# Optimization experiments

Hardware: AMD Instinct MI355X
Metric: run time of the kernel (lower is better)

## Reference

```python
import jax, jax.numpy as jnp
from jax import lax
import numpy as np


def setup_inputs() -> dict:
    key = jax.random.key(0)
    ks = iter(jax.random.split(key, 48))

    def w(shape):
        fan = shape[0] if len(shape) == 2 else int(np.prod(shape[1:]))
        return jax.random.normal(next(ks), shape, jnp.float32) / np.sqrt(fan)

    def b(n):
        return jax.random.normal(next(ks), (n,), jnp.float32) * 0.01

    T = 16
    return dict(
        search=jax.random.normal(next(ks), (3, 383, 287), jnp.float32),
        exemplars=jax.random.normal(next(ks), (T, 3, 383, 287), jnp.float32),
        # AlexNet features (random-weight stand-in for pretrained)
        aw1=w((64, 3, 11, 11)), ab1=b(64),
        aw2=w((192, 64, 5, 5)), ab2=b(192),
        aw3=w((384, 192, 3, 3)), ab3=b(384),
        aw4=w((256, 384, 3, 3)), ab4=b(256),
        aw5=w((256, 256, 3, 3)), ab5=b(256),
        # conv_deconv: Conv1d(256,256,3,p=1) -> MaxPool1d(88) -> ConvTranspose1d(256,256,88)
        wcd=w((256, 256, 3)), bcd=b(256),
        wt=w((256, 256, 88)), bt=b(256),
        # st_gcn: GCN(256, 512, 256)
        ws1=w((256, 512)), bs1=b(512),
        ws2=w((512, 256)), bs2=b(256),
        # g, h: 1x1 Conv1d(256,256) == linear maps
        wg=w((256, 256)), bg=b(256),
        wh=w((256, 256)), bh=b(256),
        # ct_gcn: GCN(256, 384, 256)
        wc1=w((256, 384)), bc1=b(384),
        wc2=w((384, 256)), bc2=b(256),
    )


def _gct_forward(search, exemplars, aw1, ab1, aw2, ab2, aw3, ab3, aw4, ab4,
                 aw5, ab5, wcd, bcd, wt, bt, ws1, bs1, ws2, bs2,
                 wg, bg, wh, bh, wc1, bc1, wc2, bc2):
    f32 = jnp.float32

    def conv2d(x, w, bias, s, p):
        y = lax.conv_general_dilated(x, w, (s, s), [(p, p), (p, p)],
                                     dimension_numbers=('NCHW', 'OIHW', 'NCHW'))
        return y + bias[None, :, None, None]

    def maxpool(x):  # k=3, s=2, VALID (AlexNet pools)
        return lax.reduce_window(x, -jnp.inf, lax.max, (1, 1, 3, 3), (1, 1, 2, 2), 'VALID')

    def features(x):
        x = maxpool(jax.nn.relu(conv2d(x, aw1, ab1, 4, 2)))
        x = maxpool(jax.nn.relu(conv2d(x, aw2, ab2, 1, 2)))
        x = jax.nn.relu(conv2d(x, aw3, ab3, 1, 1))
        x = jax.nn.relu(conv2d(x, aw4, ab4, 1, 1))
        x = maxpool(jax.nn.relu(conv2d(x, aw5, ab5, 1, 1)))
        return x

    lrelu = lambda v: jax.nn.leaky_relu(v, 0.01)

    X = features(search[None])          # [1,256,11,8]
    Z = features(exemplars)             # [T,256,11,8]
    T = Z.shape[0]
    D = X.shape[1]                      # 256
    M = X.shape[2] * X.shape[3]         # 88
    Xf = X.reshape(D, M)                # [256,88]
    Zf = Z.reshape(T, D, M)             # [T,256,88]

    # conv_deconv branch: conv1d(k=3,p=1) -> global maxpool -> conv_transpose(k=M)
    xc = lax.conv_general_dilated(Xf[None], wcd, (1,), [(1, 1)],
                                  dimension_numbers=('NCH', 'OIH', 'NCH'))[0] + bcd[:, None]
    v = jnp.max(xc, axis=1)                              # [256]
    X_hat = jnp.einsum('i,iok->ok', v, wt) + bt[:, None]  # [256,88]

    # spatiotemporal graph: A[i+T*j, i+T*k]=1 for j!=k; self-loops for t!=0
    TM = T * M
    n = jnp.arange(TM)
    same_t = (n[:, None] % T) == (n[None, :] % T)
    diff_s = (n[:, None] // T) != (n[None, :] // T)
    A1 = (same_t & diff_s).astype(f32) + jnp.diag((n % T != 0).astype(f32))

    # st GCN over TM nodes (node n = t + T*m -> spatial-major flatten)
    nodes = Zf.transpose(2, 0, 1).reshape(TM, D)          # [TM,256]
    h1 = lrelu(A1 @ (nodes @ ws1) + bs1)                  # [TM,512]
    h2 = lrelu(A1 @ (h1 @ ws2) + bs2)                     # [TM,256]
    V1 = jnp.max(h2.reshape(M, T, D), axis=1).T           # temporal max-pool -> [256,88]

    # dynamic cross-track graph: pairwise g/h affinities + row softmax (fused)
    Vx = V1 + X_hat                                       # [256,88]
    G = wg @ Vx + bg[:, None]                             # [256,88]
    Hh = wh @ Vx + bh[:, None]                            # [256,88]
    A2 = jax.nn.softmax(Hh.T @ G, axis=1)                 # [88,88], A2[j,i]=g(i).h(j)

    # ct GCN
    xv = V1.T                                             # [88,256]
    c1 = lrelu(A2 @ (xv @ wc1) + bc1)                     # [88,384]
    V2 = lrelu(A2 @ (c1 @ wc2) + bc2).T                   # [256,88]

    # F.conv2d(X[1,256,11,8], V2[1,256,11,8]) -> full-overlap correlation = scalar
    R = jnp.sum(Xf * V2).reshape(1, 1, 1, 1)
    return R


def reference(search, exemplars, aw1, ab1, aw2, ab2, aw3, ab3, aw4, ab4,
              aw5, ab5, wcd, bcd, wt, bt, ws1, bs1, ws2, bs2,
              wg, bg, wh, bh, wc1, bc1, wc2, bc2):
    return _gct_forward(search, exemplars, aw1, ab1, aw2, ab2, aw3, ab3, aw4, ab4,
                        aw5, ab5, wcd, bcd, wt, bt, ws1, bs1, ws2, bs2,
                        wg, bg, wh, bh, wc1, bc1, wc2, bc2)
```

## Files before the change

### kernel.cpp

```cpp
#include <hip/hip_runtime.h>
#include <hip/hip_bf16.h>
#include <math.h>

#define BATCH 17
#define T_EX 16
#define H0 383
#define W0 287
#define C1 64
#define H1 95
#define W1 71
#define H1P 47
#define W1P 35
#define C2 192
#define H2P 23
#define W2P 17
#define C3 384
#define C45 256
#define H5P 11
#define W5P 8
#define DD 256
#define MM 88
#define TM 1408

#define HP1 389
#define WP1 292

typedef unsigned short ushort_t;
typedef __attribute__((ext_vector_type(8))) short short8;
typedef __attribute__((ext_vector_type(4))) float f32x4;

__device__ __forceinline__ float lrelu(float v) { return v > 0.f ? v : 0.01f * v; }

__device__ __forceinline__ ushort_t f2bf(float f) {
    unsigned int u = __float_as_uint(f);
    unsigned int r = (u + 0x7fffu + ((u >> 16) & 1u)) >> 16;
    return (ushort_t)r;
}
__device__ __forceinline__ float b2f(ushort_t b) {
    return __uint_as_float(((unsigned int)b) << 16);
}
__device__ __forceinline__ short8 ld16(const ushort_t* p) { return *(const short8*)p; }
__device__ __forceinline__ short8 ld2x8(const ushort_t* p) {
    union { uint2 u[2]; short8 s; } uu;
    uu.u[0] = *(const uint2*)p;
    uu.u[1] = *(const uint2*)(p + 4);
    return uu.s;
}
__device__ __forceinline__ void async_cp16(ushort_t* l, const ushort_t* g) {
    __builtin_amdgcn_global_load_lds(
        (const __attribute__((address_space(1))) void*)g,
        (__attribute__((address_space(3))) void*)l, 16, 0, 0);
}

__global__ void zfill_k(float4* __restrict__ p, int n4) {
    int idx = blockIdx.x * 256 + threadIdx.x;
    if (idx < n4) p[idx] = (float4){0.f, 0.f, 0.f, 0.f};
}

__global__ void prep1_k(const float* __restrict__ search, const float* __restrict__ exemp,
                        ushort_t* __restrict__ out) {
    int idx = blockIdx.x * 256 + threadIdx.x;
    if (idx >= BATCH * H0 * W0) return;
    int ix = idx % W0; int t = idx / W0;
    int iy = t % H0; int b = t / H0;
    const float* src = (b == 0) ? search : exemp + (size_t)(b - 1) * 3 * H0 * W0;
    const int hw = H0 * W0;
    float v0 = src[iy * W0 + ix];
    float v1 = src[hw + iy * W0 + ix];
    float v2 = src[2 * hw + iy * W0 + ix];
    ushort4 o;
    o.x = f2bf(v0); o.y = f2bf(v1); o.z = f2bf(v2); o.w = 0;
    *(ushort4*)&out[(((size_t)b * HP1 + iy + 2) * WP1 + ix + 2) * 4] = o;
}

__global__ void wprep_k(const float* __restrict__ w, ushort_t* __restrict__ out,
                        int KH, int KWl, int KWr, int CINl, int CINr,
                        int NKS, int nch) {
    int idx = blockIdx.x * 256 + threadIdx.x;
    if (idx >= nch) return;
    int c = idx & 255;
    int rest = idx >> 8;
    int ks = rest % NKS;
    int ocb = rest / NKS;
    int k8 = c >> 6, m = c & 63;
    int oc = ocb * 64 + m;
    int KWC = KWl * CINl;
    ushort_t* o = out + (size_t)idx * 8;
#pragma unroll
    for (int j = 0; j < 8; ++j) {
        int kg = ks * 32 + k8 * 8 + j;
        int ky = kg / KWC; int rem = kg - ky * KWC;
        int kx = rem / CINl; int ic = rem - kx * CINl;
        float v = 0.f;
        if (ky < KH && kx < KWr && ic < CINr)
            v = w[(((size_t)oc * CINr + ic) * KH + ky) * KWr + kx];
        o[j] = f2bf(v);
    }
}

__global__ void wprep_gemm_k(const float* __restrict__ ws1, const float* __restrict__ ws2,
                             const float* __restrict__ wcd, ushort_t* __restrict__ WS1T,
                             ushort_t* __restrict__ WS2T, ushort_t* __restrict__ WCDT) {
    int idx = blockIdx.x * 256 + threadIdx.x;
    const float* src; ushort_t* dst; int NKS, mode = 0, sa = 1, sk = 0, base;
    if (idx < 16384)       { src = ws1; dst = WS1T; NKS = 8;  sk = 512; base = idx; }
    else if (idx < 32768)  { src = ws2; dst = WS2T; NKS = 16; sk = 256; base = idx - 16384; }
    else if (idx < 57344)  { src = wcd; dst = WCDT; NKS = 24; mode = 1; base = idx - 32768; }
    else return;
    int c = base & 255;
    int rest = base >> 8;
    int ks = rest % NKS;
    int ocb = rest / NKS;
    int k8 = c >> 6, m = c & 63;
    int oc = ocb * 64 + m;
    ushort_t* o = dst + (size_t)base * 8;
#pragma unroll
    for (int j = 0; j < 8; ++j) {
        int kg = ks * 32 + k8 * 8 + j;
        float v;
        if (mode == 0) v = src[(size_t)oc * sa + (size_t)kg * sk];
        else           v = src[(size_t)oc * 768 + (kg & 255) * 3 + (kg >> 8)];
        o[j] = f2bf(v);
    }
}

template <int STRIDE, bool A16>
__global__ __launch_bounds__(256) void conv_mfma5(
    const ushort_t* __restrict__ inp, const ushort_t* __restrict__ wt,
    const float* __restrict__ bias, ushort_t* __restrict__ out,
    int Hp, int Wp, int C, int Wout, int HW, int NKS2, int KWl,
    int OHp, int OWp, int OPAD, int COUT) {
    const int tid = threadIdx.x;
    const int wv = tid >> 6, lane = tid & 63;
    const int quad = lane >> 4, l16 = lane & 15;
    const int n_blk = blockIdx.x * 64;
    const int ocb = blockIdx.y;
    const int b = blockIdx.z;

    __shared__ ushort_t As[2][4096];
    __shared__ ushort_t Bs[2][4096];
    __shared__ int offs[432];

    const int KWC = KWl * C;
    for (int g = tid; g < NKS2 * 8; g += 256) {
        int kg = g * 8;
        int ky = kg / KWC; int rem = kg - ky * KWC;
        int kx = rem / C; int c8 = rem - kx * C;
        offs[g] = (ky * Wp + kx) * C + c8;
    }

    const ushort_t* inb = inp + (size_t)b * Hp * Wp * C;
    int n_g = n_blk + lane;
    int n_gc = n_g < HW ? n_g : HW - 1;
    int oy = n_gc / Wout, ox = n_gc - oy * Wout;
    const int base0 = (oy * STRIDE * Wp + ox * STRIDE) * C;

    f32x4 acc[4];
#pragma unroll
    for (int cn = 0; cn < 4; ++cn) acc[cn] = (f32x4){0.f, 0.f, 0.f, 0.f};

    const ushort_t* wblk = wt + (size_t)ocb * (size_t)NKS2 * 4096;

    __syncthreads();

    {
        const ushort_t* aS = wblk + tid * 8;
        async_cp16(&As[0][tid * 8], aS);
        async_cp16(&As[0][2048 + tid * 8], aS + 2048);
        const int o0 = offs[wv], o1 = offs[4 + wv];
        if (A16) {
            async_cp16(&Bs[0][tid * 8], inb + base0 + o0);
            async_cp16(&Bs[0][2048 + tid * 8], inb + base0 + o1);
        } else {
            *(short8*)&Bs[0][tid * 8] = ld2x8(inb + base0 + o0);
            *(short8*)&Bs[0][2048 + tid * 8] = ld2x8(inb + base0 + o1);
        }
    }
    __syncthreads();

    for (int ks2 = 0; ks2 < NKS2; ++ks2) {
        const int cur = ks2 & 1, nxt = cur ^ 1;
        if (ks2 + 1 < NKS2) {
            const ushort_t* aS = wblk + (size_t)(ks2 + 1) * 4096 + tid * 8;
            async_cp16(&As[nxt][tid * 8], aS);
            async_cp16(&As[nxt][2048 + tid * 8], aS + 2048);
            const int o0 = offs[(ks2 + 1) * 8 + wv], o1 = offs[(ks2 + 1) * 8 + 4 + wv];
            if (A16) {
                async_cp16(&Bs[nxt][tid * 8], inb + base0 + o0);
                async_cp16(&Bs[nxt][2048 + tid * 8], inb + base0 + o1);
            } else {
                *(short8*)&Bs[nxt][tid * 8] = ld2x8(inb + base0 + o0);
                *(short8*)&Bs[nxt][2048 + tid * 8] = ld2x8(inb + base0 + o1);
            }
        }
#pragma unroll
        for (int h = 0; h < 2; ++h) {
            const short8 af = *(const short8*)&As[cur][h * 2048 + (quad * 64 + wv * 16 + l16) * 8];
#pragma unroll
            for (int cn = 0; cn < 4; ++cn) {
                const short8 bfr = *(const short8*)&Bs[cur][h * 2048 + (quad * 64 + cn * 16 + l16) * 8];
                acc[cn] = __builtin_amdgcn_mfma_f32_16x16x32_bf16(af, bfr, acc[cn], 0, 0, 0);
            }
        }
        __syncthreads();
    }

    const int oc0 = ocb * 64 + wv * 16 + quad * 4;
    const float bi0 = bias[oc0], bi1 = bias[oc0 + 1], bi2 = bias[oc0 + 2], bi3 = bias[oc0 + 3];
#pragma unroll
    for (int cn = 0; cn < 4; ++cn) {
        int n = n_blk + cn * 16 + l16;
        if (n < HW) {
            int y = n / Wout, x = n - y * Wout;
            size_t base = (((size_t)b * OHp + y + OPAD) * OWp + x + OPAD) * COUT + oc0;
            ushort4 o;
            o.x = f2bf(fmaxf(acc[cn][0] + bi0, 0.f));
            o.y = f2bf(fmaxf(acc[cn][1] + bi1, 0.f));
            o.z = f2bf(fmaxf(acc[cn][2] + bi2, 0.f));
            o.w = f2bf(fmaxf(acc[cn][3] + bi3, 0.f));
            *(ushort4*)&out[base] = o;
        }
    }
}

template <int MODE, bool HASBIAS, bool SC1>
__global__ __launch_bounds__(256) void gemm_mfma3(
    const ushort_t* __restrict__ Bsrc, const ushort_t* __restrict__ wt,
    const float* __restrict__ bias, float* __restrict__ out,
    int RS, int N, int NKS, int sn, int sc) {
    const int tid = threadIdx.x;
    const int wv = tid >> 6, lane = tid & 63;
    const int quad = lane >> 4, l16 = lane & 15;
    const int n_blk = blockIdx.x * 64;
    const int ocb = blockIdx.y;

    __shared__ ushort_t Bs[2][2048];

    int n_g = n_blk + lane;
    int n_gc = n_g < N ? n_g : N - 1;
    int row = (MODE == 1) ? (1 + (n_gc & 15)) * MM + (n_gc >> 4) : n_gc;
    const size_t base0 = (size_t)row * RS;

    f32x4 acc[4];
#pragma unroll
    for (int cn = 0; cn < 4; ++cn) acc[cn] = (f32x4){0.f, 0.f, 0.f, 0.f};

    const ushort_t* wblk = wt + (size_t)ocb * NKS * 2048;
    const int afrag = (quad * 64 + wv * 16 + l16) * 8;

    short8 a0 = ld16(wblk + afrag);
    *(short8*)&Bs[0][tid * 8] = ld16(Bsrc + base0 + wv * 8);
    __syncthreads();

    for (int ks = 0; ks < NKS; ++ks) {
        const int cur = ks & 1, nxt = cur ^ 1;
        short8 a1, bn;
        const bool more = (ks + 1 < NKS);
        if (more) {
            a1 = ld16(wblk + (ks + 1) * 2048 + afrag);
            bn = ld16(Bsrc + base0 + (ks + 1) * 32 + wv * 8);
        }
#pragma unroll
        for (int cn = 0; cn < 4; ++cn) {
            const short8 bfr = *(const short8*)&Bs[cur][(quad * 64 + cn * 16 + l16) * 8];
            acc[cn] = __builtin_amdgcn_mfma_f32_16x16x32_bf16(a0, bfr, acc[cn], 0, 0, 0);
        }
        if (more) *(short8*)&Bs[nxt][tid * 8] = bn;
        a0 = a1;
        __syncthreads();
    }

    const int oc0 = ocb * 64 + wv * 16 + quad * 4;
    float bb[4] = {0.f, 0.f, 0.f, 0.f};
    if (HASBIAS) { bb[0] = bias[oc0]; bb[1] = bias[oc0+1]; bb[2] = bias[oc0+2]; bb[3] = bias[oc0+3]; }
#pragma unroll
    for (int cn = 0; cn < 4; ++cn) {
        int n = n_blk + cn * 16 + l16;
        if (n < N) {
            if (SC1) {
                float4 o;
                o.x = acc[cn][0] + bb[0]; o.y = acc[cn][1] + bb[1];
                o.z = acc[cn][2] + bb[2]; o.w = acc[cn][3] + bb[3];
                *(float4*)&out[(size_t)n * sn + oc0] = o;
            } else {
#pragma unroll
                for (int reg = 0; reg < 4; ++reg)
                    out[(size_t)n * sn + (size_t)(oc0 + reg) * sc] = acc[cn][reg] + bb[reg];
            }
        }
    }
}

__global__ void pool_nhwc(const ushort_t* __restrict__ in, ushort_t* __restrict__ out,
                          int C, int Hin, int Win, int Hout, int Wout,
                          int OHp, int OWp, int OPAD) {
    int total = BATCH * C * Hout * Wout;
    int idx = blockIdx.x * 256 + threadIdx.x;
    if (idx >= total) return;
    int c = idx % C; int r = idx / C;
    int x = r % Wout; r /= Wout;
    int y = r % Hout; int b = r / Hout;
    const int rs = Win * C;
    const ushort_t* p = in + (((size_t)b * Hin + 2 * y) * Win + 2 * x) * C + c;
    float m = b2f(p[0]);
    m = fmaxf(m, b2f(p[C])); m = fmaxf(m, b2f(p[2 * C]));
    m = fmaxf(m, b2f(p[rs])); m = fmaxf(m, b2f(p[rs + C])); m = fmaxf(m, b2f(p[rs + 2 * C]));
    m = fmaxf(m, b2f(p[2 * rs])); m = fmaxf(m, b2f(p[2 * rs + C])); m = fmaxf(m, b2f(p[2 * rs + 2 * C]));
    out[(((size_t)b * OHp + y + OPAD) * OWp + x + OPAD) * C + c] = f2bf(m);
}

__global__ void pool5_k(const ushort_t* __restrict__ in, float* __restrict__ P,
                        ushort_t* __restrict__ PB, ushort_t* __restrict__ XfPad) {
    int total = BATCH * 256 * MM;
    int idx = blockIdx.x * 256 + threadIdx.x;
    if (idx >= total) return;
    int c = idx % 256; int r = idx / 256;
    int x = r % W5P; r /= W5P;
    int y = r % H5P; int b = r / H5P;
    const int rs = W2P * 256;
    const ushort_t* p = in + (((size_t)b * H2P + 2 * y) * W2P + 2 * x) * 256 + c;
    float m = b2f(p[0]);
    m = fmaxf(m, b2f(p[256])); m = fmaxf(m, b2f(p[512]));
    m = fmaxf(m, b2f(p[rs])); m = fmaxf(m, b2f(p[rs + 256])); m = fmaxf(m, b2f(p[rs + 512]));
    m = fmaxf(m, b2f(p[2 * rs])); m = fmaxf(m, b2f(p[2 * rs + 256])); m = fmaxf(m, b2f(p[2 * rs + 512]));
    int mm = y * W5P + x;
    size_t o = ((size_t)b * MM + mm) * 256 + c;
    P[o] = m;
    ushort_t mb = f2bf(m);
    PB[o] = mb;
    if (b == 0) XfPad[(size_t)(mm + 1) * 256 + c] = mb;
}

__global__ void vmax_k(const float* __restrict__ xc, float* __restrict__ v) {
    int c = blockIdx.x * 64 + threadIdx.x;
    float m = -INFINITY;
    for (int j = 0; j < MM; ++j) m = fmaxf(m, xc[(size_t)c * MM + j]);
    v[c] = m;
}

__global__ void xhat_k(const float* __restrict__ v, const float* __restrict__ wt,
                       const float* __restrict__ bt, float* __restrict__ xhat) {
    __shared__ float lv[256];
    for (int j = threadIdx.x; j < 256; j += 256) lv[j] = v[j];
    __syncthreads();
    int idx = blockIdx.x * 256 + threadIdx.x;
    if (idx >= DD * MM) return;
    int k = idx % MM, o = idx / MM;
    float acc = bt[o];
    for (int i = 0; i < 256; ++i) acc = fmaf(lv[i], wt[(i * 256 + o) * MM + k], acc);
    xhat[idx] = acc;
}

__global__ void s1_k(const float* __restrict__ Y1, float* __restrict__ S1) {
    int idx = blockIdx.x * 256 + threadIdx.x;
    if (idx >= T_EX * 512) return;
    int c = idx % 512, t = idx / 512;
    float acc = 0.f;
    for (int m = 0; m < MM; ++m) acc += Y1[(m * T_EX + t) * 512 + c];
    S1[idx] = acc;
}

__global__ void h1_k(const float* __restrict__ Y1, const float* __restrict__ S1,
                     const float* __restrict__ bs1, ushort_t* __restrict__ h1b) {
    int idx = blockIdx.x * 256 + threadIdx.x;
    if (idx >= TM * 512) return;
    int c = idx % 512; int n = idx / 512;
    int t = n % T_EX;
    float val = S1[t * 512 + c] + bs1[c];
    if (t == 0) val -= Y1[idx];
    h1b[idx] = f2bf(lrelu(val));
}

__global__ void s2_k(const float* __restrict__ Y2, float* __restrict__ S2) {
    int idx = blockIdx.x * 256 + threadIdx.x;
    if (idx >= T_EX * 256) return;
    int c = idx % 256, t = idx / 256;
    float acc = 0.f;
    for (int m = 0; m < MM; ++m) acc += Y2[(m * T_EX + t) * 256 + c];
    S2[idx] = acc;
}

__global__ void h2_k(const float* __restrict__ Y2, const float* __restrict__ S2,
                     const float* __restrict__ bs2, float* __restrict__ h2) {
    int idx = blockIdx.x * 256 + threadIdx.x;
    if (idx >= TM * 256) return;
    int c = idx % 256; int n = idx / 256;
    int t = n % T_EX;
    float val = S2[t * 256 + c] + bs2[c];
    if (t == 0) val -= Y2[idx];
    h2[idx] = lrelu(val);
}

__global__ void v1vx_k(const float* __restrict__ h2, const float* __restrict__ xhat,
                       float* __restrict__ V1, float* __restrict__ Vx) {
    int idx = blockIdx.x * 256 + threadIdx.x;
    if (idx >= DD * MM) return;
    int m = idx % MM, d = idx / MM;
    float mx = -INFINITY;
    for (int t = 0; t < T_EX; ++t) mx = fmaxf(mx, h2[(m * T_EX + t) * 256 + d]);
    V1[idx] = mx;
    Vx[idx] = mx + xhat[idx];
}

__global__ void lin88_k(const float* __restrict__ Wg, const float* __restrict__ bg,
                        const float* __restrict__ Wh, const float* __restrict__ bh,
                        const float* __restrict__ Vin, float* __restrict__ Gout,
                        float* __restrict__ Hout) {
    int idx = blockIdx.x * 256 + threadIdx.x;
    if (idx >= DD * MM) return;
    const float* W = blockIdx.y ? Wh : Wg;
    const float* bias = blockIdx.y ? bh : bg;
    float* out = blockIdx.y ? Hout : Gout;
    int m = idx % MM, o = idx / MM;
    const float* wr = W + o * 256;
    float acc = bias[o];
    for (int i = 0; i < 256; ++i) acc = fmaf(wr[i], Vin[i * MM + m], acc);
    out[idx] = acc;
}

__global__ void smsm_k(const float* __restrict__ Hh, const float* __restrict__ G,
                       float* __restrict__ A2) {
    int j = blockIdx.x;
    int tid = threadIdx.x;
    __shared__ float row[96];
    __shared__ float red[128];
    for (int i = tid; i < MM; i += 128) {
        float acc = 0.f;
        for (int c = 0; c < 256; ++c) acc = fmaf(Hh[c * MM + j], G[c * MM + i], acc);
        row[i] = acc;
    }
    __syncthreads();
    float val = (tid < MM) ? row[tid] : -INFINITY;
    red[tid] = val; __syncthreads();
    for (int s = 64; s > 0; s >>= 1) {
        if (tid < s) red[tid] = fmaxf(red[tid], red[tid + s]);
        __syncthreads();
    }
    float mx = red[0]; __syncthreads();
    float e = (tid < MM) ? expf(val - mx) : 0.f;
    red[tid] = e; __syncthreads();
    for (int s = 64; s > 0; s >>= 1) {
        if (tid < s) red[tid] += red[tid + s];
        __syncthreads();
    }
    float inv = 1.f / red[0];
    if (tid < MM) A2[j * MM + tid] = e * inv;
}

__global__ void t1_k(const float* __restrict__ V1, const float* __restrict__ wc1,
                     float* __restrict__ t1) {
    int idx = blockIdx.x * 256 + threadIdx.x;
    if (idx >= MM * 384) return;
    int c = idx % 384, m = idx / 384;
    float acc = 0.f;
    for (int d = 0; d < 256; ++d) acc = fmaf(V1[d * MM + m], wc1[d * 384 + c], acc);
    t1[idx] = acc;
}

__global__ void c1_k(const float* __restrict__ A2, const float* __restrict__ t1,
                     const float* __restrict__ bc1, float* __restrict__ c1) {
    int idx = blockIdx.x * 256 + threadIdx.x;
    if (idx >= MM * 384) return;
    int c = idx % 384, j = idx / 384;
    float acc = bc1[c];
    for (int i = 0; i < MM; ++i) acc = fmaf(A2[j * MM + i], t1[i * 384 + c], acc);
    c1[idx] = lrelu(acc);
}

__global__ void t2_k(const float* __restrict__ c1, const float* __restrict__ wc2,
                     float* __restrict__ t2) {
    int idx = blockIdx.x * 256 + threadIdx.x;
    if (idx >= MM * 256) return;
    int c = idx % 256, m = idx / 256;
    const float* cr = c1 + m * 384;
    float acc = 0.f;
    for (int d = 0; d < 384; ++d) acc = fmaf(cr[d], wc2[d * 256 + c], acc);
    t2[idx] = acc;
}

__global__ void v2_k(const float* __restrict__ A2, const float* __restrict__ t2,
                     const float* __restrict__ bc2, float* __restrict__ V2m) {
    int idx = blockIdx.x * 256 + threadIdx.x;
    if (idx >= MM * 256) return;
    int c = idx % 256, j = idx / 256;
    float acc = bc2[c];
    for (int i = 0; i < MM; ++i) acc = fmaf(A2[j * MM + i], t2[i * 256 + c], acc);
    V2m[idx] = lrelu(acc);
}

__global__ void final_k(const float* __restrict__ Xf2, const float* __restrict__ V2m,
                        float* __restrict__ out) {
    __shared__ float red[256];
    float acc = 0.f;
    for (int idx = threadIdx.x; idx < DD * MM; idx += 256)
        acc = fmaf(Xf2[idx], V2m[idx], acc);
    red[threadIdx.x] = acc; __syncthreads();
    for (int s = 128; s > 0; s >>= 1) {
        if (threadIdx.x < s) red[threadIdx.x] += red[threadIdx.x + s];
        __syncthreads();
    }
    if (threadIdx.x == 0) out[0] = red[0];
}

extern "C" void kernel_launch(void* const* d_in, const int* in_sizes, int n_in,
                              void* d_out, int out_size, void* d_ws, size_t ws_size,
                              hipStream_t stream) {
    const float* search = (const float*)d_in[0];
    const float* exemp  = (const float*)d_in[1];
    const float* aw1 = (const float*)d_in[2];  const float* ab1 = (const float*)d_in[3];
    const float* aw2 = (const float*)d_in[4];  const float* ab2 = (const float*)d_in[5];
    const float* aw3 = (const float*)d_in[6];  const float* ab3 = (const float*)d_in[7];
    const float* aw4 = (const float*)d_in[8];  const float* ab4 = (const float*)d_in[9];
    const float* aw5 = (const float*)d_in[10]; const float* ab5 = (const float*)d_in[11];
    const float* wcd = (const float*)d_in[12]; const float* bcd = (const float*)d_in[13];
    const float* wt  = (const float*)d_in[14]; const float* bt  = (const float*)d_in[15];
    const float* ws1 = (const float*)d_in[16]; const float* bs1 = (const float*)d_in[17];
    const float* ws2 = (const float*)d_in[18]; const float* bs2 = (const float*)d_in[19];
    const float* wg  = (const float*)d_in[20]; const float* bg  = (const float*)d_in[21];
    const float* wh  = (const float*)d_in[22]; const float* bh  = (const float*)d_in[23];
    const float* wc1 = (const float*)d_in[24]; const float* bc1 = (const float*)d_in[25];
    const float* wc2 = (const float*)d_in[26]; const float* bc2 = (const float*)d_in[27];

    float* ws = (float*)d_ws;
    float* R1 = ws;
    float* R2 = ws + 3870720;
    float* R3 = ws + 7544832;
    float* Wg = ws + 8628864;

    ushort_t* in1p  = (ushort_t*)R1;
    ushort_t* c1out = (ushort_t*)R2;
    ushort_t* p1out = (ushort_t*)R3;
    ushort_t* c2out = (ushort_t*)R1;
    ushort_t* p2out = (ushort_t*)R2;
    ushort_t* c3out = (ushort_t*)(R2 + 775200);
    ushort_t* c4out = (ushort_t*)R1;
    ushort_t* c5out = (ushort_t*)R3;
    ushort_t* WT    = (ushort_t*)Wg;

    zfill_k<<<(965500 + 255) / 256, 256, 0, stream>>>((float4*)R1, 965500);
    prep1_k<<<(BATCH * H0 * W0 + 255) / 256, 256, 0, stream>>>(search, exemp, in1p);
    wprep_k<<<(4608 + 255) / 256, 256, 0, stream>>>(aw1, WT, 11, 12, 11, 4, 3, 18, 4608);
    conv_mfma5<4, false><<<dim3(106, 1, BATCH), 256, 0, stream>>>(
        in1p, WT, ab1, c1out, HP1, WP1, 4, W1, H1 * W1, 9, 12, H1, W1, 0, 64);
    zfill_k<<<(270504 + 255) / 256, 256, 0, stream>>>((float4*)R3, 270504);
    pool_nhwc<<<(BATCH * 64 * H1P * W1P + 255) / 256, 256, 0, stream>>>(
        c1out, p1out, 64, H1, W1, H1P, W1P, 51, 39, 2);
    wprep_k<<<(38400 + 255) / 256, 256, 0, stream>>>(aw2, WT, 5, 5, 5, 64, 64, 50, 38400);
    conv_mfma5<1, true><<<dim3(26, 3, BATCH), 256, 0, stream>>>(
        p1out, WT, ab2, c2out, 51, 39, 64, W1P, H1P * W1P, 25, 5, H1P, W1P, 0, 192);
    zfill_k<<<(581400 + 255) / 256, 256, 0, stream>>>((float4*)R2, 581400);
    pool_nhwc<<<(BATCH * 192 * H2P * W2P + 255) / 256, 256, 0, stream>>>(
        c2out, p2out, 192, H1P, W1P, H2P, W2P, 25, 19, 1);
    wprep_k<<<(82944 + 255) / 256, 256, 0, stream>>>(aw3, WT, 3, 3, 3, 192, 192, 54, 82944);
    conv_mfma5<1, true><<<dim3(7, 6, BATCH), 256, 0, stream>>>(
        p2out, WT, ab3, c3out, 25, 19, 192, W2P, H2P * W2P, 27, 3, 25, 19, 1, 384);
    zfill_k<<<(258400 + 255) / 256, 256, 0, stream>>>((float4*)R1, 258400);
    wprep_k<<<(110592 + 255) / 256, 256, 0, stream>>>(aw4, WT, 3, 3, 3, 384, 384, 108, 110592);
    conv_mfma5<1, true><<<dim3(7, 4, BATCH), 256, 0, stream>>>(
        c3out, WT, ab4, c4out, 25, 19, 384, W2P, H2P * W2P, 54, 3, 25, 19, 1, 256);
    wprep_k<<<(73728 + 255) / 256, 256, 0, stream>>>(aw5, WT, 3, 3, 3, 256, 256, 72, 73728);
    conv_mfma5<1, true><<<dim3(7, 4, BATCH), 256, 0, stream>>>(
        c4out, WT, ab5, c5out, 25, 19, 256, W2P, H2P * W2P, 36, 3, H2P, W2P, 0, 256);

    float*    P      = R1 + 2417664;
    ushort_t* PB     = (ushort_t*)(R1 + 2800640);
    ushort_t* XfPad  = (ushort_t*)(R1 + 2992128);
    float*    xc     = R1 + 3003648;

    ushort_t* WS1T = (ushort_t*)Wg;
    ushort_t* WS2T = (ushort_t*)(Wg + 65536);
    ushort_t* WCDT = (ushort_t*)(Wg + 131072);
    wprep_gemm_k<<<(57344 + 255) / 256, 256, 0, stream>>>(ws1, ws2, wcd, WS1T, WS2T, WCDT);

    pool5_k<<<(BATCH * 256 * MM + 255) / 256, 256, 0, stream>>>(c5out, P, PB, XfPad);
    float* Xf2 = P;

    float* v_   = R1 + 0;
    float* xhat = R1 + 1024;
    float* Y1   = R1 + 23552;
    float* S1   = R1 + 744448;
    ushort_t* h1b = (ushort_t*)(R1 + 752640);
    float* Y2   = R1 + 1473536;
    float* S2   = R1 + 1833984;
    float* h2   = R1 + 1838080;
    float* V1   = R1 + 2198528;
    float* Vx   = R1 + 2221056;
    float* G    = R1 + 2243584;
    float* Hh   = R1 + 2266112;
    float* A2   = R1 + 2296832;
    float* t1   = R1 + 2305024;
    float* c1   = R1 + 2338816;
    float* t2   = R1 + 2372608;
    float* V2m  = R1 + 2395136;

    gemm_mfma3<0, true, false><<<dim3(2, 4), 256, 0, stream>>>(
        XfPad, WCDT, bcd, xc, 256, MM, 24, 1, MM);
    vmax_k<<<4, 64, 0, stream>>>(xc, v_);
    xhat_k<<<(DD * MM + 255) / 256, 256, 0, stream>>>(v_, wt, bt, xhat);

    gemm_mfma3<1, false, true><<<dim3(22, 8), 256, 0, stream>>>(
        PB, WS1T, nullptr, Y1, 256, TM, 8, 512, 1);
    s1_k<<<(T_EX * 512 + 255) / 256, 256, 0, stream>>>(Y1, S1);
    h1_k<<<(TM * 512 + 255) / 256, 256, 0, stream>>>(Y1, S1, bs1, h1b);
    gemm_mfma3<0, false, true><<<dim3(22, 4), 256, 0, stream>>>(
        h1b, WS2T, nullptr, Y2, 512, TM, 16, 256, 1);
    s2_k<<<(T_EX * 256 + 255) / 256, 256, 0, stream>>>(Y2, S2);
    h2_k<<<(TM * 256 + 255) / 256, 256, 0, stream>>>(Y2, S2, bs2, h2);
    v1vx_k<<<(DD * MM + 255) / 256, 256, 0, stream>>>(h2, xhat, V1, Vx);

    lin88_k<<<dim3((DD * MM + 255) / 256, 2), 256, 0, stream>>>(wg, bg, wh, bh, Vx, G, Hh);
    smsm_k<<<MM, 128, 0, stream>>>(Hh, G, A2);

    t1_k<<<(MM * 384 + 255) / 256, 256, 0, stream>>>(V1, wc1, t1);
    c1_k<<<(MM * 384 + 255) / 256, 256, 0, stream>>>(A2, t1, bc1, c1);
    t2_k<<<(MM * 256 + 255) / 256, 256, 0, stream>>>(c1, wc2, t2);
    v2_k<<<(MM * 256 + 255) / 256, 256, 0, stream>>>(A2, t2, bc2, V2m);

    final_k<<<1, 256, 0, stream>>>(Xf2, V2m, (float*)d_out);
}
```

Before: 547.6 us.

## Widen conv MFMA tiles to 64x128 and flatten batch into pixel dimension

The implicit-GEMM conv kernel now computes a 64-channel by 128-pixel tile per block, with each wave holding a 2x4 grid of accumulators, so every A fragment is reused across more MFMAs. The batch dimension is folded into the pixel index, which removes partial tiles at per-image boundaries and gives a flat grid. All B loads now go through async global-to-LDS copies, including the stride-4 first conv that previously used register loads, and syncthreads is replaced by explicit vmcnt waits and raw barriers. The cost is more registers and LDS per block and fewer blocks for the small late layers.

Result: slower. 591.5 us (+8.0%).

```diff
diff --git a/kernel.cpp b/kernel.cpp
--- a/kernel.cpp
+++ b/kernel.cpp
@@ -40,12 +40,6 @@
     return __uint_as_float(((unsigned int)b) << 16);
 }
 __device__ __forceinline__ short8 ld16(const ushort_t* p) { return *(const short8*)p; }
-__device__ __forceinline__ short8 ld2x8(const ushort_t* p) {
-    union { uint2 u[2]; short8 s; } uu;
-    uu.u[0] = *(const uint2*)p;
-    uu.u[1] = *(const uint2*)(p + 4);
-    return uu.s;
-}
 __device__ __forceinline__ void async_cp16(ushort_t* l, const ushort_t* g) {
     __builtin_amdgcn_global_load_lds(
         (const __attribute__((address_space(1))) void*)g,
@@ -124,21 +118,21 @@
     }
 }
 
-template <int STRIDE, bool A16>
-__global__ __launch_bounds__(256) void conv_mfma5(
+template <int STRIDE>
+__global__ __launch_bounds__(256) void conv_mfma6(
     const ushort_t* __restrict__ inp, const ushort_t* __restrict__ wt,
     const float* __restrict__ bias, ushort_t* __restrict__ out,
-    int Hp, int Wp, int C, int Wout, int HW, int NKS2, int KWl,
+    int Hp, int Wp, int C, int Wout, int HW, int Ntot, int NKS2, int KWl,
     int OHp, int OWp, int OPAD, int COUT) {
     const int tid = threadIdx.x;
     const int wv = tid >> 6, lane = tid & 63;
     const int quad = lane >> 4, l16 = lane & 15;
-    const int n_blk = blockIdx.x * 64;
+    const int wr = wv >> 1, wc = wv & 1;
+    const int n_blk = blockIdx.x * 128;
     const int ocb = blockIdx.y;
-    const int b = blockIdx.z;
 
     __shared__ ushort_t As[2][4096];
-    __shared__ ushort_t Bs[2][4096];
+    __shared__ ushort_t Bs[2][8192];
     __shared__ int offs[432];
 
     const int KWC = KWl * C;
@@ -149,15 +143,21 @@
         offs[g] = (ky * Wp + kx) * C + c8;
     }
 
-    const ushort_t* inb = inp + (size_t)b * Hp * Wp * C;
-    int n_g = n_blk + lane;
-    int n_gc = n_g < HW ? n_g : HW - 1;
-    int oy = n_gc / Wout, ox = n_gc - oy * Wout;
-    const int base0 = (oy * STRIDE * Wp + ox * STRIDE) * C;
-
-    f32x4 acc[4];
-#pragma unroll
-    for (int cn = 0; cn < 4; ++cn) acc[cn] = (f32x4){0.f, 0.f, 0.f, 0.f};
+    int n0 = n_blk + lane;      if (n0 >= Ntot) n0 = Ntot - 1;
+    int n1 = n_blk + 64 + lane; if (n1 >= Ntot) n1 = Ntot - 1;
+    const int b0 = n0 / HW, p0 = n0 - b0 * HW;
+    const int b1 = n1 / HW, p1 = n1 - b1 * HW;
+    const int oy0 = p0 / Wout, ox0 = p0 - oy0 * Wout;
+    const int oy1 = p1 / Wout, ox1 = p1 - oy1 * Wout;
+    const size_t HWC = (size_t)Hp * Wp * C;
+    const ushort_t* src0 = inp + (size_t)b0 * HWC + (size_t)(oy0 * STRIDE * Wp + ox0 * STRIDE) * C;
+    const ushort_t* src1 = inp + (size_t)b1 * HWC + (size_t)(oy1 * STRIDE * Wp + ox1 * STRIDE) * C;
+
+    f32x4 acc[2][4];
+#pragma unroll
+    for (int m = 0; m < 2; ++m)
+#pragma unroll
+        for (int n = 0; n < 4; ++n) acc[m][n] = (f32x4){0.f, 0.f, 0.f, 0.f};
 
     const ushort_t* wblk = wt + (size_t)ocb * (size_t)NKS2 * 4096;
 
@@ -168,57 +168,65 @@
         async_cp16(&As[0][tid * 8], aS);
         async_cp16(&As[0][2048 + tid * 8], aS + 2048);
         const int o0 = offs[wv], o1 = offs[4 + wv];
-        if (A16) {
-            async_cp16(&Bs[0][tid * 8], inb + base0 + o0);
-            async_cp16(&Bs[0][2048 + tid * 8], inb + base0 + o1);
-        } else {
-            *(short8*)&Bs[0][tid * 8] = ld2x8(inb + base0 + o0);
-            *(short8*)&Bs[0][2048 + tid * 8] = ld2x8(inb + base0 + o1);
-        }
-    }
-    __syncthreads();
+        ushort_t* bb = &Bs[0][wv * 512 + lane * 8];
+        async_cp16(bb,        src0 + o0);
+        async_cp16(bb + 2048, src1 + o0);
+        async_cp16(bb + 4096, src0 + o1);
+        async_cp16(bb + 6144, src1 + o1);
+    }
 
     for (int ks2 = 0; ks2 < NKS2; ++ks2) {
-        const int cur = ks2 & 1, nxt = cur ^ 1;
+        const int cur = ks2 & 1;
         if (ks2 + 1 < NKS2) {
+            const int nxt = cur ^ 1;
             const ushort_t* aS = wblk + (size_t)(ks2 + 1) * 4096 + tid * 8;
             async_cp16(&As[nxt][tid * 8], aS);
             async_cp16(&As[nxt][2048 + tid * 8], aS + 2048);
             const int o0 = offs[(ks2 + 1) * 8 + wv], o1 = offs[(ks2 + 1) * 8 + 4 + wv];
-            if (A16) {
-                async_cp16(&Bs[nxt][tid * 8], inb + base0 + o0);
-                async_cp16(&Bs[nxt][2048 + tid * 8], inb + base0 + o1);
-            } else {
-                *(short8*)&Bs[nxt][tid * 8] = ld2x8(inb + base0 + o0);
-                *(short8*)&Bs[nxt][2048 + tid * 8] = ld2x8(inb + base0 + o1);
+            ushort_t* bb = &Bs[nxt][wv * 512 + lane * 8];
+            async_cp16(bb,        src0 + o0);
+            async_cp16(bb + 2048, src1 + o0);
+            async_cp16(bb + 4096, src0 + o1);
+            async_cp16(bb + 6144, src1 + o1);
+            asm volatile("s_waitcnt vmcnt(6)");
+        } else {
+            asm volatile("s_waitcnt vmcnt(0)");
+        }
+        __builtin_amdgcn_s_barrier();
+        __builtin_amdgcn_sched_barrier(0);
+#pragma unroll
+        for (int h = 0; h < 2; ++h) {
+            const short8 a0 = *(const short8*)&As[cur][h * 2048 + (quad * 64 + wr * 32 + l16) * 8];
+            const short8 a1 = *(const short8*)&As[cur][h * 2048 + (quad * 64 + wr * 32 + 16 + l16) * 8];
+#pragma unroll
+            for (int n = 0; n < 4; ++n) {
+                const short8 bfr = *(const short8*)&Bs[cur][h * 4096 + wc * 2048 + (quad * 64 + n * 16 + l16) * 8];
+                acc[0][n] = __builtin_amdgcn_mfma_f32_16x16x32_bf16(a0, bfr, acc[0][n], 0, 0, 0);
+                acc[1][n] = __builtin_amdgcn_mfma_f32_16x16x32_bf16(a1, bfr, acc[1][n], 0, 0, 0);
             }
         }
-#pragma unroll
-        for (int h = 0; h < 2; ++h) {
-            const short8 af = *(const short8*)&As[cur][h * 2048 + (quad * 64 + wv * 16 + l16) * 8];
-#pragma unroll
-            for (int cn = 0; cn < 4; ++cn) {
-                const short8 bfr = *(const short8*)&Bs[cur][h * 2048 + (quad * 64 + cn * 16 + l16) * 8];
-                acc[cn] = __builtin_amdgcn_mfma_f32_16x16x32_bf16(af, bfr, acc[cn], 0, 0, 0);
+        __builtin_amdgcn_sched_barrier(0);
+        __builtin_amdgcn_s_barrier();
+    }
+
+    const int oc0 = ocb * 64 + wr * 32 + quad * 4;
+#pragma unroll
+    for (int n = 0; n < 4; ++n) {
+        int npx = n_blk + wc * 64 + n * 16 + l16;
+        if (npx < Ntot) {
+            int bb = npx / HW; int pix = npx - bb * HW;
+            int y = pix / Wout, x = pix - y * Wout;
+            size_t basep = (((size_t)bb * OHp + y + OPAD) * OWp + x + OPAD) * COUT;
+#pragma unroll
+            for (int m = 0; m < 2; ++m) {
+                const int oc = oc0 + m * 16;
+                ushort4 o;
+                o.x = f2bf(fmaxf(acc[m][n][0] + bias[oc], 0.f));
+                o.y = f2bf(fmaxf(acc[m][n][1] + bias[oc + 1], 0.f));
+                o.z = f2bf(fmaxf(acc[m][n][2] + bias[oc + 2], 0.f));
+                o.w = f2bf(fmaxf(acc[m][n][3] + bias[oc + 3], 0.f));
+                *(ushort4*)&out[basep + oc] = o;
             }
-        }
-        __syncthreads();
-    }
-
-    const int oc0 = ocb * 64 + wv * 16 + quad * 4;
-    const float bi0 = bias[oc0], bi1 = bias[oc0 + 1], bi2 = bias[oc0 + 2], bi3 = bias[oc0 + 3];
-#pragma unroll
-    for (int cn = 0; cn < 4; ++cn) {
-        int n = n_blk + cn * 16 + l16;
-        if (n < HW) {
-            int y = n / Wout, x = n - y * Wout;
-            size_t base = (((size_t)b * OHp + y + OPAD) * OWp + x + OPAD) * COUT + oc0;
-            ushort4 o;
-            o.x = f2bf(fmaxf(acc[cn][0] + bi0, 0.f));
-            o.y = f2bf(fmaxf(acc[cn][1] + bi1, 0.f));
-            o.z = f2bf(fmaxf(acc[cn][2] + bi2, 0.f));
-            o.w = f2bf(fmaxf(acc[cn][3] + bi3, 0.f));
-            *(ushort4*)&out[base] = o;
         }
     }
 }
@@ -540,27 +548,27 @@
     zfill_k<<<(965500 + 255) / 256, 256, 0, stream>>>((float4*)R1, 965500);
     prep1_k<<<(BATCH * H0 * W0 + 255) / 256, 256, 0, stream>>>(search, exemp, in1p);
     wprep_k<<<(4608 + 255) / 256, 256, 0, stream>>>(aw1, WT, 11, 12, 11, 4, 3, 18, 4608);
-    conv_mfma5<4, false><<<dim3(106, 1, BATCH), 256, 0, stream>>>(
-        in1p, WT, ab1, c1out, HP1, WP1, 4, W1, H1 * W1, 9, 12, H1, W1, 0, 64);
+    conv_mfma6<4><<<dim3(896, 1), 256, 0, stream>>>(
+        in1p, WT, ab1, c1out, HP1, WP1, 4, W1, H1 * W1, BATCH * H1 * W1, 9, 12, H1, W1, 0, 64);
     zfill_k<<<(270504 + 255) / 256, 256, 0, stream>>>((float4*)R3, 270504);
     pool_nhwc<<<(BATCH * 64 * H1P * W1P + 255) / 256, 256, 0, stream>>>(
         c1out, p1out, 64, H1, W1, H1P, W1P, 51, 39, 2);
     wprep_k<<<(38400 + 255) / 256, 256, 0, stream>>>(aw2, WT, 5, 5, 5, 64, 64, 50, 38400);
-    conv_mfma5<1, true><<<dim3(26, 3, BATCH), 256, 0, stream>>>(
-        p1out, WT, ab2, c2out, 51, 39, 64, W1P, H1P * W1P, 25, 5, H1P, W1P, 0, 192);
+    conv_mfma6<1><<<dim3(219, 3), 256, 0, stream>>>(
+        p1out, WT, ab2, c2out, 51, 39, 64, W1P, H1P * W1P, BATCH * H1P * W1P, 25, 5, H1P, W1P, 0, 192);
     zfill_k<<<(581400 + 255) / 256, 256, 0, stream>>>((float4*)R2, 581400);
     pool_nhwc<<<(BATCH * 192 * H2P * W2P + 255) / 256, 256, 0, stream>>>(
         c2out, p2out, 192, H1P, W1P, H2P, W2P, 25, 19, 1);
     wprep_k<<<(82944 + 255) / 256, 256, 0, stream>>>(aw3, WT, 3, 3, 3, 192, 192, 54, 82944);
-    conv_mfma5<1, true><<<dim3(7, 6, BATCH), 256, 0, stream>>>(
-        p2out, WT, ab3, c3out, 25, 19, 192, W2P, H2P * W2P, 27, 3, 25, 19, 1, 384);
+    conv_mfma6<1><<<dim3(52, 6), 256, 0, stream>>>(
+        p2out, WT, ab3, c3out, 25, 19, 192, W2P, H2P * W2P, BATCH * H2P * W2P, 27, 3, 25, 19, 1, 384);
     zfill_k<<<(258400 + 255) / 256, 256, 0, stream>>>((float4*)R1, 258400);
     wprep_k<<<(110592 + 255) / 256, 256, 0, stream>>>(aw4, WT, 3, 3, 3, 384, 384, 108, 110592);
-    conv_mfma5<1, true><<<dim3(7, 4, BATCH), 256, 0, stream>>>(
-        c3out, WT, ab4, c4out, 25, 19, 384, W2P, H2P * W2P, 54, 3, 25, 19, 1, 256);
+    conv_mfma6<1><<<dim3(52, 4), 256, 0, stream>>>(
+        c3out, WT, ab4, c4out, 25, 19, 384, W2P, H2P * W2P, BATCH * H2P * W2P, 54, 3, 25, 19, 1, 256);
     wprep_k<<<(73728 + 255) / 256, 256, 0, stream>>>(aw5, WT, 3, 3, 3, 256, 256, 72, 73728);
-    conv_mfma5<1, true><<<dim3(7, 4, BATCH), 256, 0, stream>>>(
-        c4out, WT, ab5, c5out, 25, 19, 256, W2P, H2P * W2P, 36, 3, H2P, W2P, 0, 256);
+    conv_mfma6<1><<<dim3(52, 4), 256, 0, stream>>>(
+        c4out, WT, ab5, c5out, 25, 19, 256, W2P, H2P * W2P, BATCH * H2P * W2P, 36, 3, H2P, W2P, 0, 256);
 
     float*    P      = R1 + 2417664;
     ushort_t* PB     = (ushort_t*)(R1 + 2800640);
```

## Flatten batch into GEMM N and stream conv weights directly into registers

Applied to the files above, without the earlier changes.

The implicit-GEMM conv kernel now folds the batch dimension into the pixel dimension, so tiles no longer waste lanes on each image's partial last tile. Weight fragments are loaded straight from global memory into registers instead of being staged through LDS. The double-buffered input pipeline is rebuilt with explicit vmcnt waits, raw s_barriers and sched_barriers. Conv1 also switches to the async global-to-LDS path that was previously reserved for the other layers. The goal is less LDS traffic, fewer wasted tiles and better load/MFMA overlap. The cost is exposed global latency on the register weight loads and fragile hand-written wait counts.

New measurement: 555.6 us. Within noise of the previous version (+1.5%).

```diff
diff --git a/kernel.cpp b/kernel.cpp
--- a/kernel.cpp
+++ b/kernel.cpp
@@ -40,12 +40,6 @@
     return __uint_as_float(((unsigned int)b) << 16);
 }
 __device__ __forceinline__ short8 ld16(const ushort_t* p) { return *(const short8*)p; }
-__device__ __forceinline__ short8 ld2x8(const ushort_t* p) {
-    union { uint2 u[2]; short8 s; } uu;
-    uu.u[0] = *(const uint2*)p;
-    uu.u[1] = *(const uint2*)(p + 4);
-    return uu.s;
-}
 __device__ __forceinline__ void async_cp16(ushort_t* l, const ushort_t* g) {
     __builtin_amdgcn_global_load_lds(
         (const __attribute__((address_space(1))) void*)g,
@@ -124,20 +118,18 @@
     }
 }
 
-template <int STRIDE, bool A16>
-__global__ __launch_bounds__(256) void conv_mfma5(
+template <int STRIDE>
+__global__ __launch_bounds__(256) void conv_mfma7(
     const ushort_t* __restrict__ inp, const ushort_t* __restrict__ wt,
     const float* __restrict__ bias, ushort_t* __restrict__ out,
-    int Hp, int Wp, int C, int Wout, int HW, int NKS2, int KWl,
+    int Hp, int Wp, int C, int Wout, int HW, int Ntot, int NKS2, int KWl,
     int OHp, int OWp, int OPAD, int COUT) {
     const int tid = threadIdx.x;
     const int wv = tid >> 6, lane = tid & 63;
     const int quad = lane >> 4, l16 = lane & 15;
     const int n_blk = blockIdx.x * 64;
     const int ocb = blockIdx.y;
-    const int b = blockIdx.z;
-
-    __shared__ ushort_t As[2][4096];
+
     __shared__ ushort_t Bs[2][4096];
     __shared__ int offs[432];
 
@@ -149,60 +141,58 @@
         offs[g] = (ky * Wp + kx) * C + c8;
     }
 
-    const ushort_t* inb = inp + (size_t)b * Hp * Wp * C;
-    int n_g = n_blk + lane;
-    int n_gc = n_g < HW ? n_g : HW - 1;
-    int oy = n_gc / Wout, ox = n_gc - oy * Wout;
-    const int base0 = (oy * STRIDE * Wp + ox * STRIDE) * C;
+    int n0 = n_blk + lane; if (n0 >= Ntot) n0 = Ntot - 1;
+    const int b0 = n0 / HW, p0 = n0 - b0 * HW;
+    const int oy0 = p0 / Wout, ox0 = p0 - oy0 * Wout;
+    const ushort_t* src0 = inp + (size_t)b0 * Hp * Wp * C +
+                           (size_t)(oy0 * STRIDE * Wp + ox0 * STRIDE) * C;
 
     f32x4 acc[4];
 #pragma unroll
     for (int cn = 0; cn < 4; ++cn) acc[cn] = (f32x4){0.f, 0.f, 0.f, 0.f};
 
     const ushort_t* wblk = wt + (size_t)ocb * (size_t)NKS2 * 4096;
+    const ushort_t* wp = wblk + (size_t)(quad * 64 + wv * 16 + l16) * 8;
 
     __syncthreads();
 
     {
-        const ushort_t* aS = wblk + tid * 8;
-        async_cp16(&As[0][tid * 8], aS);
-        async_cp16(&As[0][2048 + tid * 8], aS + 2048);
         const int o0 = offs[wv], o1 = offs[4 + wv];
-        if (A16) {
-            async_cp16(&Bs[0][tid * 8], inb + base0 + o0);
-            async_cp16(&Bs[0][2048 + tid * 8], inb + base0 + o1);
+        async_cp16(&Bs[0][tid * 8], src0 + o0);
+        async_cp16(&Bs[0][2048 + tid * 8], src0 + o1);
+    }
+    short8 ac0 = ld16(wp);
+    short8 ac1 = ld16(wp + 2048);
+
+    for (int ks2 = 0; ks2 < NKS2; ++ks2) {
+        const int cur = ks2 & 1;
+        if (ks2 + 1 < NKS2) {
+            const int o0 = offs[(ks2 + 1) * 8 + wv], o1 = offs[(ks2 + 1) * 8 + 4 + wv];
+            ushort_t* bb = &Bs[cur ^ 1][0];
+            async_cp16(bb + tid * 8, src0 + o0);
+            async_cp16(bb + 2048 + tid * 8, src0 + o1);
+            asm volatile("s_waitcnt vmcnt(2)");
         } else {
-            *(short8*)&Bs[0][tid * 8] = ld2x8(inb + base0 + o0);
-            *(short8*)&Bs[0][2048 + tid * 8] = ld2x8(inb + base0 + o1);
+            asm volatile("s_waitcnt vmcnt(0)");
         }
-    }
-    __syncthreads();
-
-    for (int ks2 = 0; ks2 < NKS2; ++ks2) {
-        const int cur = ks2 & 1, nxt = cur ^ 1;
-        if (ks2 + 1 < NKS2) {
-            const ushort_t* aS = wblk + (size_t)(ks2 + 1) * 4096 + tid * 8;
-            async_cp16(&As[nxt][tid * 8], aS);
-            async_cp16(&As[nxt][2048 + tid * 8], aS + 2048);
-            const int o0 = offs[(ks2 + 1) * 8 + wv], o1 = offs[(ks2 + 1) * 8 + 4 + wv];
-            if (A16) {
-                async_cp16(&Bs[nxt][tid * 8], inb + base0 + o0);
-                async_cp16(&Bs[nxt][2048 + tid * 8], inb + base0 + o1);
-            } else {
-                *(short8*)&Bs[nxt][tid * 8] = ld2x8(inb + base0 + o0);
-                *(short8*)&Bs[nxt][2048 + tid * 8] = ld2x8(inb + base0 + o1);
-            }
-        }
+        __builtin_amdgcn_s_barrier();
+        __builtin_amdgcn_sched_barrier(0);
 #pragma unroll
         for (int h = 0; h < 2; ++h) {
-            const short8 af = *(const short8*)&As[cur][h * 2048 + (quad * 64 + wv * 16 + l16) * 8];
+            const short8 af = h ? ac1 : ac0;
 #pragma unroll
             for (int cn = 0; cn < 4; ++cn) {
                 const short8 bfr = *(const short8*)&Bs[cur][h * 2048 + (quad * 64 + cn * 16 + l16) * 8];
                 acc[cn] = __builtin_amdgcn_mfma_f32_16x16x32_bf16(af, bfr, acc[cn], 0, 0, 0);
             }
         }
-        __syncthreads();
+        __builtin_amdgcn_sched_barrier(0);
+        __builtin_amdgcn_s_barrier();
+        if (ks2 + 1 < NKS2) {
+            const ushort_t* wp2 = wp + (size_t)(ks2 + 1) * 4096;
+            ac0 = ld16(wp2);
+            ac1 = ld16(wp2 + 2048);
+        }
     }
 
     const int oc0 = ocb * 64 + wv * 16 + quad * 4;
@@ -210,9 +200,10 @@
 #pragma unroll
     for (int cn = 0; cn < 4; ++cn) {
         int n = n_blk + cn * 16 + l16;
-        if (n < HW) {
-            int y = n / Wout, x = n - y * Wout;
-            size_t base = (((size_t)b * OHp + y + OPAD) * OWp + x + OPAD) * COUT + oc0;
+        if (n < Ntot) {
+            int bb = n / HW; int pix = n - bb * HW;
+            int y = pix / Wout, x = pix - y * Wout;
+            size_t base = (((size_t)bb * OHp + y + OPAD) * OWp + x + OPAD) * COUT + oc0;
             ushort4 o;
             o.x = f2bf(fmaxf(acc[cn][0] + bi0, 0.f));
             o.y = f2bf(fmaxf(acc[cn][1] + bi1, 0.f));
@@ -540,27 +531,27 @@
     zfill_k<<<(965500 + 255) / 256, 256, 0, stream>>>((float4*)R1, 965500);
     prep1_k<<<(BATCH * H0 * W0 + 255) / 256, 256, 0, stream>>>(search, exemp, in1p);
     wprep_k<<<(4608 + 255) / 256, 256, 0, stream>>>(aw1, WT, 11, 12, 11, 4, 3, 18, 4608);
-    conv_mfma5<4, false><<<dim3(106, 1, BATCH), 256, 0, stream>>>(
-        in1p, WT, ab1, c1out, HP1, WP1, 4, W1, H1 * W1, 9, 12, H1, W1, 0, 64);
+    conv_mfma7<4><<<dim3(1792, 1), 256, 0, stream>>>(
+        in1p, WT, ab1, c1out, HP1, WP1, 4, W1, H1 * W1, BATCH * H1 * W1, 9, 12, H1, W1, 0, 64);
     zfill_k<<<(270504 + 255) / 256, 256, 0, stream>>>((float4*)R3, 270504);
     pool_nhwc<<<(BATCH * 64 * H1P * W1P + 255) / 256, 256, 0, stream>>>(
         c1out, p1out, 64, H1, W1, H1P, W1P, 51, 39, 2);
     wprep_k<<<(38400 + 255) / 256, 256, 0, stream>>>(aw2, WT, 5, 5, 5, 64, 64, 50, 38400);
-    conv_mfma5<1, true><<<dim3(26, 3, BATCH), 256, 0, stream>>>(
-        p1out, WT, ab2, c2out, 51, 39, 64, W1P, H1P * W1P, 25, 5, H1P, W1P, 0, 192);
+    conv_mfma7<1><<<dim3(437, 3), 256, 0, stream>>>(
+        p1out, WT, ab2, c2out, 51, 39, 64, W1P, H1P * W1P, BATCH * H1P * W1P, 25, 5, H1P, W1P, 0, 192);
     zfill_k<<<(581400 + 255) / 256, 256, 0, stream>>>((float4*)R2, 581400);
     pool_nhwc<<<(BATCH * 192 * H2P * W2P + 255) / 256, 256, 0, stream>>>(
         c2out, p2out, 192, H1P, W1P, H2P, W2P, 25, 19, 1);
     wprep_k<<<(82944 + 255) / 256, 256, 0, stream>>>(aw3, WT, 3, 3, 3, 192, 192, 54, 82944);
-    conv_mfma5<1, true><<<dim3(7, 6, BATCH), 256, 0, stream>>>(
-        p2out, WT, ab3, c3out, 25, 19, 192, W2P, H2P * W2P, 27, 3, 25, 19, 1, 384);
+    conv_mfma7<1><<<dim3(104, 6), 256, 0, stream>>>(
+        p2out, WT, ab3, c3out, 25, 19, 192, W2P, H2P * W2P, BATCH * H2P * W2P, 27, 3, 25, 19, 1, 384);
     zfill_k<<<(258400 + 255) / 256, 256, 0, stream>>>((float4*)R1, 258400);
     wprep_k<<<(110592 + 255) / 256, 256, 0, stream>>>(aw4, WT, 3, 3, 3, 384, 384, 108, 110592);
-    conv_mfma5<1, true><<<dim3(7, 4, BATCH), 256, 0, stream>>>(
-        c3out, WT, ab4, c4out, 25, 19, 384, W2P, H2P * W2P, 54, 3, 25, 19, 1, 256);
+    conv_mfma7<1><<<dim3(104, 4), 256, 0, stream>>>(
+        c3out, WT, ab4, c4out, 25, 19, 384, W2P, H2P * W2P, BATCH * H2P * W2P, 54, 3, 25, 19, 1, 256);
     wprep_k<<<(73728 + 255) / 256, 256, 0, stream>>>(aw5, WT, 3, 3, 3, 256, 256, 72, 73728);
-    conv_mfma5<1, true><<<dim3(7, 4, BATCH), 256, 0, stream>>>(
-        c4out, WT, ab5, c5out, 25, 19, 256, W2P, H2P * W2P, 36, 3, H2P, W2P, 0, 256);
+    conv_mfma7<1><<<dim3(104, 4), 256, 0, stream>>>(
+        c4out, WT, ab5, c5out, 25, 19, 256, W2P, H2P * W2P, BATCH * H2P * W2P, 36, 3, H2P, W2P, 0, 256);
 
     float*    P      = R1 + 2417664;
     ushort_t* PB     = (ushort_t*)(R1 + 2800640);
```
